# Optimization experiments

Hardware: AMD Instinct MI355X
Metric: run time of the kernel (lower is better)

The kernel has to match this reference:

```python
import jax, jax.numpy as jnp
import numpy as np

N_QUBITS = 4
N_LAYERS = 2
PI_CONST = 3.1415  # matches torch code's literal
C64 = jnp.complex64

# CNOT as a (2,2,2,2) tensor: indices (c_out, t_out, c_in, t_in)
_CNOT = jnp.array([[1,0,0,0],[0,1,0,0],[0,0,0,1],[0,0,1,0]], dtype=C64).reshape(2,2,2,2)

def _m2(a, b, c, d):
    return jnp.stack([jnp.stack([a, b]), jnp.stack([c, d])]).astype(C64)

def _rx(t):
    c = jnp.cos(t / 2).astype(C64); s = jnp.sin(t / 2).astype(C64)
    return _m2(c, -1j * s, -1j * s, c)

def _ry(t):
    c = jnp.cos(t / 2).astype(C64); s = jnp.sin(t / 2).astype(C64)
    return _m2(c, -s, s, c)

def _rz(t):
    t = t.astype(C64)
    e = jnp.exp(-1j * t / 2)
    z = jnp.zeros((), C64)
    return _m2(e, z, z, jnp.conj(e))

def _apply1(state, U, w):
    st = jnp.tensordot(U, state, axes=([1], [w]))
    return jnp.moveaxis(st, 0, w)

def _apply_cnot(state, c, t):
    st = jnp.tensordot(_CNOT, state, axes=([2, 3], [c, t]))
    return jnp.moveaxis(st, [0, 1], [c, t])

def _circuit(xin, weights):
    # xin: (4,) angles; weights: (L, 4, 3)
    state = jnp.zeros((2,) * N_QUBITS, C64).reshape(-1).at[0].set(1.0).reshape((2,) * N_QUBITS)
    for q in range(N_QUBITS):
        state = _apply1(state, _ry(xin[q]), q)
    for layer in range(weights.shape[0]):
        for q in range(N_QUBITS):
            state = _apply1(state, _rx(weights[layer, q, 0]), q)
            state = _apply1(state, _ry(weights[layer, q, 1]), q)
            state = _apply1(state, _rz(weights[layer, q, 2]), q)
        for q in range(N_QUBITS - 1):
            state = _apply_cnot(state, q, q + 1)
    p = state.real ** 2 + state.imag ** 2  # (2,2,2,2) probabilities
    evs = []
    for q in range(N_QUBITS):
        pq = p.sum(axis=tuple(a for a in range(N_QUBITS) if a != q))  # (2,)
        evs.append(pq[0] - pq[1])
    return jnp.stack(evs)  # (4,)

def setup_inputs() -> dict:
    key = jax.random.key(0)
    kx, kw = jax.random.split(key)
    x = jax.random.normal(kx, (1048576, 8), dtype=jnp.float32)
    weights = 0.01 * jax.random.normal(kw, (N_LAYERS, N_QUBITS, 3), dtype=jnp.float32)
    return {"x": x, "weights": weights}

def reference(x, weights):
    # pad/truncate to n_qubits (here: truncate, feat=8 > 4)
    x_in = jnp.tanh(x[:, :N_QUBITS]) * PI_CONST  # (B, 4)
    return jax.vmap(_circuit, in_axes=(0, None))(x_in, weights)  # (B, 4)
```

## Files before the change

### kernel.cpp

```cpp
#include <hip/hip_runtime.h>
#include <hip/hip_bf16.h>


__global__ __launch_bounds__(256) void qsetup(const float* __restrict__ w,
                                              float* __restrict__ C) {
    __shared__ float Ur[16][16];
    __shared__ float Ui[16][16];
    __shared__ float M[16][16];
    const int q = blockIdx.x;
    const int tid = threadIdx.x;

    if (tid < 16) {
        float re[16], im[16];
#pragma unroll
        for (int i = 0; i < 16; ++i) { re[i] = (i == tid) ? 1.0f : 0.0f; im[i] = 0.0f; }

#pragma unroll
        for (int ly = 0; ly < 2; ++ly) {
#pragma unroll
            for (int qq = 0; qq < 4; ++qq) {
                const int mm = 8 >> qq;
                float th, c, s;
                th = w[(ly * 4 + qq) * 3 + 0] * 0.5f; c = __cosf(th); s = __sinf(th);
#pragma unroll
                for (int i = 0; i < 16; ++i) if (!(i & mm)) {
                    const int j = i | mm;
                    float r0 = re[i], i0 = im[i], r1 = re[j], i1 = im[j];
                    re[i] = c * r0 + s * i1;  im[i] = c * i0 - s * r1;
                    re[j] = s * i0 + c * r1;  im[j] = -s * r0 + c * i1;
                }
                th = w[(ly * 4 + qq) * 3 + 1] * 0.5f; c = __cosf(th); s = __sinf(th);
#pragma unroll
                for (int i = 0; i < 16; ++i) if (!(i & mm)) {
                    const int j = i | mm;
                    float r0 = re[i], i0 = im[i], r1 = re[j], i1 = im[j];
                    re[i] = c * r0 - s * r1;  im[i] = c * i0 - s * i1;
                    re[j] = s * r0 + c * r1;  im[j] = s * i0 + c * i1;
                }
                th = w[(ly * 4 + qq) * 3 + 2] * 0.5f; c = __cosf(th); s = __sinf(th);
#pragma unroll
                for (int i = 0; i < 16; ++i) if (!(i & mm)) {
                    const int j = i | mm;
                    float r0 = re[i], i0 = im[i], r1 = re[j], i1 = im[j];
                    re[i] = c * r0 + s * i0;  im[i] = c * i0 - s * r0;
                    re[j] = c * r1 - s * i1;  im[j] = c * i1 + s * r1;
                }
            }
#pragma unroll
            for (int qq = 0; qq < 3; ++qq) {
                const int mc = 8 >> qq, mt = 8 >> (qq + 1);
#pragma unroll
                for (int i = 0; i < 16; ++i) if ((i & mc) && !(i & mt)) {
                    const int j = i | mt;
                    float tr = re[i]; re[i] = re[j]; re[j] = tr;
                    float ti = im[i]; im[i] = im[j]; im[j] = ti;
                }
            }
        }
#pragma unroll
        for (int k = 0; k < 16; ++k) { Ur[k][tid] = re[k]; Ui[k][tid] = im[k]; }
    }
    __syncthreads();

    {
        const int j = tid >> 4, l = tid & 15;
        float acc = 0.0f;
#pragma unroll
        for (int k = 0; k < 16; ++k) {
            const float sgn = ((k >> (3 - q)) & 1) ? -1.0f : 1.0f;
            acc += sgn * (Ur[k][j] * Ur[k][l] + Ui[k][j] * Ui[k][l]);
        }
        M[j][l] = acc;
    }
    __syncthreads();

    if (tid < 81) {
        int ap[4];
        ap[0] = tid / 27; ap[1] = (tid / 9) % 3; ap[2] = (tid / 3) % 3; ap[3] = tid % 3;
        float acc = 0.0f;
        for (int m = 0; m < 16; ++m) {
            int j = 0, l = 0; float sgn = 1.0f;
#pragma unroll
            for (int p = 0; p < 4; ++p) {
                const int o = (m >> (3 - p)) & 1;
                int jb = o, lb = (ap[p] == 2) ? (o ^ 1) : o;
                if (ap[p] == 1 && o) sgn = -sgn;
                j = (j << 1) | jb; l = (l << 1) | lb;
            }
            acc += sgn * M[j][l];
        }
        C[q * 81 + tid] = acc * 0.0625f;
    }
}

#define ELEMS_PER_THREAD 4

__global__ __launch_bounds__(256) void qmain(const float* __restrict__ x,
                                             const float* __restrict__ C,
                                             float* __restrict__ out, int B) {
    const int tid = blockIdx.x * 256 + threadIdx.x;
    const int total = gridDim.x * 256;

    float cg[ELEMS_PER_THREAD][4], sg[ELEMS_PER_THREAD][4];
    bool valid[ELEMS_PER_THREAD];
#pragma unroll
    for (int k = 0; k < ELEMS_PER_THREAD; ++k) {
        const int b = tid + k * total;
        valid[k] = (b < B);
        float4 xv = make_float4(0.f, 0.f, 0.f, 0.f);
        if (valid[k]) xv = *reinterpret_cast<const float4*>(x + (size_t)b * 8);
        float xs[4] = {xv.x, xv.y, xv.z, xv.w};
#pragma unroll
        for (int q = 0; q < 4; ++q) {
            const float e = __expf(2.0f * xs[q]);
            const float t = 1.0f - __fdividef(2.0f, e + 1.0f);
            const float th = 3.1415f * t;
            cg[k][q] = __cosf(th);
            sg[k][q] = __sinf(th);
        }
    }

#pragma unroll
    for (int k = 0; k < ELEMS_PER_THREAD; ++k) {
        if (!valid[k]) continue;
        const int b = tid + k * total;
        float ev[4];
#pragma unroll
        for (int q = 0; q < 4; ++q) {
            const float* __restrict__ Cq = C + q * 81;
            float r27[27];
#pragma unroll
            for (int m = 0; m < 27; ++m)
                r27[m] = Cq[3 * m] + Cq[3 * m + 1] * cg[k][3] + Cq[3 * m + 2] * sg[k][3];
            float r9[9];
#pragma unroll
            for (int m = 0; m < 9; ++m)
                r9[m] = r27[3 * m] + r27[3 * m + 1] * cg[k][2] + r27[3 * m + 2] * sg[k][2];
            float r3[3];
#pragma unroll
            for (int m = 0; m < 3; ++m)
                r3[m] = r9[3 * m] + r9[3 * m + 1] * cg[k][1] + r9[3 * m + 2] * sg[k][1];
            ev[q] = r3[0] + r3[1] * cg[k][0] + r3[2] * sg[k][0];
        }
        *reinterpret_cast<float4*>(out + (size_t)b * 4) =
            make_float4(ev[0], ev[1], ev[2], ev[3]);
    }
}

extern "C" void kernel_launch(void* const* d_in, const int* in_sizes, int n_in,
                              void* d_out, int out_size, void* d_ws, size_t ws_size,
                              hipStream_t stream) {
    const float* x = (const float*)d_in[0];
    const float* w = (const float*)d_in[1];
    float* out = (float*)d_out;
    float* C = (float*)d_ws;

    const int B = in_sizes[0] / 8;

    qsetup<<<4, 256, 0, stream>>>(w, C);

    const int ept = ELEMS_PER_THREAD;
    const int threads_needed = (B + ept - 1) / ept;
    const int grid = (threads_needed + 255) / 256;
    qmain<<<grid, 256, 0, stream>>>(x, C, out, B);
}
```

Baseline: 29.61 us.

## Stage coefficient table in LDS and interleave elements per coefficient load

Each block copies the 324-float coefficient table into shared memory, and the contraction loop is restructured so every loaded coefficient is reused across all elements a thread handles, written with explicit FMAs. Elements per thread drop from 4 to 2, doubling the grid. The goal is to replace repeated scalar global loads of C with LDS reads and gain more parallelism, at the cost of a block-wide barrier and higher register pressure from the interleaved intermediate arrays.

```diff
diff --git a/kernel.cpp b/kernel.cpp
--- a/kernel.cpp
+++ b/kernel.cpp
@@ -93,18 +93,22 @@
     }
 }
 
-#define ELEMS_PER_THREAD 4
+#define EPT 2
 
 __global__ __launch_bounds__(256) void qmain(const float* __restrict__ x,
                                              const float* __restrict__ C,
                                              float* __restrict__ out, int B) {
+    __shared__ float sC[324];
+    for (int i = threadIdx.x; i < 324; i += 256) sC[i] = C[i];
+    __syncthreads();
+
     const int tid = blockIdx.x * 256 + threadIdx.x;
     const int total = gridDim.x * 256;
 
-    float cg[ELEMS_PER_THREAD][4], sg[ELEMS_PER_THREAD][4];
-    bool valid[ELEMS_PER_THREAD];
+    float cg[EPT][4], sg[EPT][4];
+    bool valid[EPT];
 #pragma unroll
-    for (int k = 0; k < ELEMS_PER_THREAD; ++k) {
+    for (int k = 0; k < EPT; ++k) {
         const int b = tid + k * total;
         valid[k] = (b < B);
         float4 xv = make_float4(0.f, 0.f, 0.f, 0.f);
@@ -120,30 +124,44 @@
         }
     }
 
+    float ev[EPT][4];
 #pragma unroll
-    for (int k = 0; k < ELEMS_PER_THREAD; ++k) {
-        if (!valid[k]) continue;
+    for (int q = 0; q < 4; ++q) {
+        const float* __restrict__ Cq = sC + q * 81;
+        float r27[EPT][27];
+#pragma unroll
+        for (int m = 0; m < 27; ++m) {
+            const float c0 = Cq[3 * m], c1 = Cq[3 * m + 1], c2 = Cq[3 * m + 2];
+#pragma unroll
+            for (int k = 0; k < EPT; ++k)
+                r27[k][m] = __fmaf_rn(c2, sg[k][3], __fmaf_rn(c1, cg[k][3], c0));
+        }
+        float r9[EPT][9];
+#pragma unroll
+        for (int m = 0; m < 9; ++m)
+#pragma unroll
+            for (int k = 0; k < EPT; ++k)
+                r9[k][m] = __fmaf_rn(r27[k][3 * m + 2], sg[k][2],
+                           __fmaf_rn(r27[k][3 * m + 1], cg[k][2], r27[k][3 * m]));
+        float r3[EPT][3];
+#pragma unroll
+        for (int m = 0; m < 3; ++m)
+#pragma unroll
+            for (int k = 0; k < EPT; ++k)
+                r3[k][m] = __fmaf_rn(r9[k][3 * m + 2], sg[k][1],
+                           __fmaf_rn(r9[k][3 * m + 1], cg[k][1], r9[k][3 * m]));
+#pragma unroll
+        for (int k = 0; k < EPT; ++k)
+            ev[k][q] = __fmaf_rn(r3[k][2], sg[k][0],
+                       __fmaf_rn(r3[k][1], cg[k][0], r3[k][0]));
+    }
+
+#pragma unroll
+    for (int k = 0; k < EPT; ++k) {
         const int b = tid + k * total;
-        float ev[4];
-#pragma unroll
-        for (int q = 0; q < 4; ++q) {
-            const float* __restrict__ Cq = C + q * 81;
-            float r27[27];
-#pragma unroll
-            for (int m = 0; m < 27; ++m)
-                r27[m] = Cq[3 * m] + Cq[3 * m + 1] * cg[k][3] + Cq[3 * m + 2] * sg[k][3];
-            float r9[9];
-#pragma unroll
-            for (int m = 0; m < 9; ++m)
-                r9[m] = r27[3 * m] + r27[3 * m + 1] * cg[k][2] + r27[3 * m + 2] * sg[k][2];
-            float r3[3];
-#pragma unroll
-            for (int m = 0; m < 3; ++m)
-                r3[m] = r9[3 * m] + r9[3 * m + 1] * cg[k][1] + r9[3 * m + 2] * sg[k][1];
-            ev[q] = r3[0] + r3[1] * cg[k][0] + r3[2] * sg[k][0];
-        }
-        *reinterpret_cast<float4*>(out + (size_t)b * 4) =
-            make_float4(ev[0], ev[1], ev[2], ev[3]);
+        if (valid[k])
+            *reinterpret_cast<float4*>(out + (size_t)b * 4) =
+                make_float4(ev[k][0], ev[k][1], ev[k][2], ev[k][3]);
     }
 }
 
@@ -159,8 +177,7 @@
 
     qsetup<<<4, 256, 0, stream>>>(w, C);
 
-    const int ept = ELEMS_PER_THREAD;
-    const int threads_needed = (B + ept - 1) / ept;
+    const int threads_needed = (B + EPT - 1) / EPT;
     const int grid = (threads_needed + 255) / 256;
     qmain<<<grid, 256, 0, stream>>>(x, C, out, B);
 }
```

New measurement: 44.01 us. 48.6% more time.
